# Kernel optimization log

Measured on AMD Instinct MI355X. Metric: run time of the kernel, lower is better.

The kernel has to match this reference:

```python
import jax, jax.numpy as jnp
import numpy as np

VOCAB = 65
N_EMBED = 256
BLOCK = 32
N_HEAD = 4
N_BLOCKS = 8
HEAD_DIM = N_EMBED // N_HEAD          # 64 (actual projection size)
SCALE = 32 ** (-0.5)                   # source bug: scales by GLOBAL head_size=32
LN_EPS = 1e-5


def _layer_norm(x, g, b):
    m = jnp.mean(x, axis=-1, keepdims=True)
    v = jnp.mean((x - m) ** 2, axis=-1, keepdims=True)
    return (x - m) * jax.lax.rsqrt(v + LN_EPS) * g + b


def setup_inputs() -> dict:
    key = jax.random.key(0)
    ks = jax.random.split(key, 24)
    B, T = 4096, 32
    s = 0.02
    inp = {
        "x": jax.random.randint(ks[0], (B, T), 0, VOCAB),
        "y": jax.random.randint(ks[1], (B, T), 0, VOCAB),
        "tok_table": jax.random.normal(ks[2], (VOCAB, N_EMBED)) * s,
        "pos_table": jax.random.normal(ks[3], (VOCAB, N_EMBED)) * s,
        "Wk": jax.random.normal(ks[4], (N_BLOCKS, N_HEAD, N_EMBED, HEAD_DIM)) * s,
        "Wq": jax.random.normal(ks[5], (N_BLOCKS, N_HEAD, N_EMBED, HEAD_DIM)) * s,
        "Wv": jax.random.normal(ks[6], (N_BLOCKS, N_HEAD, N_EMBED, HEAD_DIM)) * s,
        "Wp": jax.random.normal(ks[7], (N_BLOCKS, N_EMBED, N_EMBED)) * s,
        "bp": jnp.zeros((N_BLOCKS, N_EMBED)),
        "ln1g": jnp.ones((N_BLOCKS, N_EMBED)),
        "ln1b": jnp.zeros((N_BLOCKS, N_EMBED)),
        "W1": jax.random.normal(ks[8], (N_BLOCKS, N_EMBED, 4 * N_EMBED)) * s,
        "b1": jnp.zeros((N_BLOCKS, 4 * N_EMBED)),
        "W2": jax.random.normal(ks[9], (N_BLOCKS, 4 * N_EMBED, N_EMBED)) * s,
        "b2": jnp.zeros((N_BLOCKS, N_EMBED)),
        "ln2g": jnp.ones((N_BLOCKS, N_EMBED)),
        "ln2b": jnp.zeros((N_BLOCKS, N_EMBED)),
        "lmW": jax.random.normal(ks[10], (N_EMBED, VOCAB)) * s,
        "lmb": jnp.zeros((VOCAB,)),
    }
    return inp


def reference(x, y, tok_table, pos_table, Wk, Wq, Wv, Wp, bp, ln1g, ln1b,
              W1, b1, W2, b2, ln2g, ln2b, lmW, lmb):
    B, T = x.shape
    # NOTE: the source indexes the position table with TOKEN ids (a bug we preserve)
    h = tok_table[x] + pos_table[x]                       # [B,T,C]
    tril = jnp.tril(jnp.ones((T, T), dtype=bool))         # [T,T]

    for i in range(N_BLOCKS):
        # --- multi-head attention (scores = k @ q^T, per source) ---
        k = jnp.einsum('btc,hcd->bhtd', h, Wk[i])
        q = jnp.einsum('btc,hcd->bhtd', h, Wq[i])
        v = jnp.einsum('btc,hcd->bhtd', h, Wv[i])
        wei = jnp.einsum('bhtd,bhsd->bhts', k, q) * SCALE  # [B,H,T,T]
        wei = jnp.where(tril[None, None], wei, -jnp.inf)
        wei = jax.nn.softmax(wei, axis=-1)
        attn = jnp.einsum('bhts,bhsd->bhtd', wei, v)       # [B,H,T,Dh]
        attn = attn.transpose(0, 2, 1, 3).reshape(B, T, N_EMBED)
        attn = attn @ Wp[i] + bp[i]
        h = _layer_norm(h + attn, ln1g[i], ln1b[i])
        # --- feed-forward ---
        ff = jax.nn.relu(h @ W1[i] + b1[i]) @ W2[i] + b2[i]
        h = _layer_norm(h + ff, ln2g[i], ln2b[i])

    logits = h @ lmW + lmb                                 # [B,T,V]
    logp = jax.nn.log_softmax(logits, axis=-1)
    loss = -jnp.mean(jnp.take_along_axis(logp, y[..., None], axis=-1))
    return logits, loss
```

## Files before the change

kernel.cpp:

```cpp
#include <hip/hip_runtime.h>
#include <hip/hip_bf16.h>

#define M_TOTAL 131072
#define ATT_SCALE 0.17677669529663687f
#define LN_EPS 1e-5f
#define CDIV(a,b) (((a)+(b)-1)/(b))

using bf16x8 = __attribute__((ext_vector_type(8))) short;
using f32x4  = __attribute__((ext_vector_type(4))) float;

__device__ __forceinline__ float wredsum(float v){
#pragma unroll
  for (int m = 32; m; m >>= 1) v += __shfl_xor(v, m, 64);
  return v;
}

__device__ __forceinline__ unsigned short f2b(float x){
  union { float f; unsigned u; } v; v.f = x;
  unsigned r = v.u + 0x7FFFu + ((v.u >> 16) & 1u);
  return (unsigned short)(r >> 16);
}
__device__ __forceinline__ float b2f(unsigned short u){
  union { unsigned u32; float f; } v; v.u32 = (unsigned)u << 16; return v.f;
}

__global__ void zero1(float* p){ if (threadIdx.x == 0) *p = 0.f; }

__global__ void convert_qkv(const float* __restrict__ Wk, const float* __restrict__ Wq,
                            const float* __restrict__ Wv, unsigned short* __restrict__ WrT){
  int idx = blockIdx.x * 256 + threadIdx.x;
  if (idx >= 8 * 768 * 256) return;
  int k = idx & 255;
  int n = (idx >> 8) % 768;
  int i = idx / (768 * 256);
  int sel = n >> 8, nn = n & 255, hh = nn >> 6, d = nn & 63;
  const float* W = sel == 0 ? Wk : sel == 1 ? Wq : Wv;
  WrT[idx] = f2b(W[((size_t)(i * 4 + hh) * 256 + k) * 64 + d]);
}

__global__ void convert_t(const float* __restrict__ in, unsigned short* __restrict__ outp,
                          int N, int K, int total){
  int idx = blockIdx.x * 256 + threadIdx.x;
  if (idx >= total) return;
  int k = idx % K;
  int n = (idx / K) % N;
  int i = idx / (K * N);
  outp[idx] = f2b(in[((size_t)i * K + k) * N + n]);
}

__global__ void convert_lmw(const float* __restrict__ lmW, const float* __restrict__ lmb,
                            unsigned short* __restrict__ lmWT, float* __restrict__ lmbp){
  int idx = blockIdx.x * 256 + threadIdx.x;
  if (idx >= 80 * 256) return;
  int k = idx & 255, c = idx >> 8;
  lmWT[idx] = (c < 65) ? f2b(lmW[k * 65 + c]) : (unsigned short)0;
  if (idx < 80) lmbp[idx] = (idx < 65) ? lmb[idx] : 0.f;
}

template<bool RELU>
__global__ __launch_bounds__(256)
void gemm_bf(const unsigned short* __restrict__ A, const unsigned short* __restrict__ BT,
             const float* __restrict__ bias, unsigned short* __restrict__ Cb,
             int N, int K){
  __shared__ __align__(16) unsigned short LDS[2][128][64];
  unsigned short (*As)[64] = LDS[0];
  unsigned short (*Bs)[64] = LDS[1];
  const int tid = threadIdx.x;
  const int rowBase = blockIdx.y * 128, colBase = blockIdx.x * 128;
  const int w = tid >> 6, lane = tid & 63;
  const int wm = w >> 1, wn = w & 1;
  const int lm = lane & 15, lk = lane >> 4;

  const int sgrow = w * 32 + (lane >> 3);
  const int sgcol = ((((lane & 7) * 16) ^ ((lane >> 3) << 4)) >> 1);
  const unsigned short* gA = A  + (size_t)(rowBase + sgrow) * K + sgcol;
  const unsigned short* gB = BT + (size_t)(colBase + sgrow) * K + sgcol;

  f32x4 acc[4][4];
#pragma unroll
  for (int m = 0; m < 4; ++m)
#pragma unroll
    for (int n = 0; n < 4; ++n) acc[m][n] = (f32x4){0.f, 0.f, 0.f, 0.f};

  for (int kt = 0; kt < K; kt += 64){
#pragma unroll
    for (int q = 0; q < 4; ++q){
      __builtin_amdgcn_global_load_lds(
        (const __attribute__((address_space(1))) void*)(gA + (size_t)(q * 8) * K + kt),
        (__attribute__((address_space(3))) void*)&As[w * 32 + q * 8][0], 16, 0, 0);
      __builtin_amdgcn_global_load_lds(
        (const __attribute__((address_space(1))) void*)(gB + (size_t)(q * 8) * K + kt),
        (__attribute__((address_space(3))) void*)&Bs[w * 32 + q * 8][0], 16, 0, 0);
    }
    __syncthreads();
#pragma unroll
    for (int half = 0; half < 2; ++half){
      const int cb = (half * 64 + lk * 16) ^ ((lm & 7) << 4);
      bf16x8 a[4], b[4];
#pragma unroll
      for (int m = 0; m < 4; ++m)
        a[m] = *(const bf16x8*)((const char*)&As[wm * 64 + m * 16 + lm][0] + cb);
#pragma unroll
      for (int n = 0; n < 4; ++n)
        b[n] = *(const bf16x8*)((const char*)&Bs[wn * 64 + n * 16 + lm][0] + cb);
#pragma unroll
      for (int m = 0; m < 4; ++m)
#pragma unroll
        for (int n = 0; n < 4; ++n)
          acc[m][n] = __builtin_amdgcn_mfma_f32_16x16x32_bf16(a[m], b[n], acc[m][n], 0, 0, 0);
    }
    __syncthreads();
  }

  unsigned short* bounce = &LDS[0][0][0] + w * 1152;
  const int erow = lane >> 2;
  const int ecol = (lane & 3) * 16;
  const int gc = colBase + wn * 64 + ecol;
#pragma unroll
  for (int m = 0; m < 4; ++m){
#pragma unroll
    for (int n = 0; n < 4; ++n){
      int c = colBase + wn * 64 + n * 16 + lm;
      float bv = bias ? bias[c] : 0.f;
#pragma unroll
      for (int i = 0; i < 4; ++i){
        float v = acc[m][n][i] + bv;
        if (RELU) v = fmaxf(v, 0.f);
        bounce[(lk * 4 + i) * 72 + n * 16 + lm] = f2b(v);
      }
    }
    asm volatile("s_waitcnt lgkmcnt(0)" ::: "memory");
    uint4 v0 = *(const uint4*)&bounce[erow * 72 + ecol];
    uint4 v1 = *(const uint4*)&bounce[erow * 72 + ecol + 8];
    size_t go = (size_t)(rowBase + wm * 64 + m * 16 + erow) * N + gc;
    *(uint4*)(Cb + go)     = v0;
    *(uint4*)(Cb + go + 8) = v1;
  }
}

__global__ void embed_kernel(const int* __restrict__ x, const float* __restrict__ tok,
                             const float* __restrict__ pos, unsigned short* __restrict__ h_bf,
                             int row0, int nrows){
  int total = nrows * 64;
  for (int idx = blockIdx.x * blockDim.x + threadIdx.x; idx < total; idx += gridDim.x * blockDim.x){
    int r = idx >> 6, c4 = (idx & 63) * 4;
    int t = x[row0 + r];
    float4 tv = *(const float4*)(tok + t * 256 + c4);
    float4 pv = *(const float4*)(pos + t * 256 + c4);
    ushort4 o;
    o.x = f2b(tv.x + pv.x); o.y = f2b(tv.y + pv.y);
    o.z = f2b(tv.z + pv.z); o.w = f2b(tv.w + pv.w);
    *(ushort4*)(h_bf + (size_t)r * 256 + c4) = o;
  }
}

__global__ __launch_bounds__(256)
void attn_mfma(const unsigned short* __restrict__ kqv, unsigned short* __restrict__ attn){
  __shared__ __align__(16) unsigned short VT[4][64 * 40];
  __shared__ __align__(16) unsigned short PH[4][32 * 40];
  const int ls = blockIdx.x;
  const int tid = threadIdx.x;
  const int hd = tid >> 6, lane = tid & 63;
  const int lm = lane & 15, lk = lane >> 4;

#pragma unroll
  for (int it = 0; it < 4; ++it){
    int idx = it * 256 + tid;
    int row = idx & 31, col = (idx >> 5) * 8;
    int hh = col >> 6, d = col & 63;
    union { uint4 v4; unsigned short s[8]; } u;
    u.v4 = *(const uint4*)(kqv + (size_t)(ls * 32 + row) * 768 + 512 + col);
#pragma unroll
    for (int j = 0; j < 8; ++j)
      VT[hh][(d + j) * 40 + row] = u.s[j];
  }
  __syncthreads();

  const unsigned short* Kg = kqv + (size_t)(ls * 32) * 768 + hd * 64;
  const unsigned short* Qg = Kg + 256;
  f32x4 sacc[2][2];
#pragma unroll
  for (int m = 0; m < 2; ++m)
#pragma unroll
    for (int n = 0; n < 2; ++n) sacc[m][n] = (f32x4){0.f, 0.f, 0.f, 0.f};
#pragma unroll
  for (int kk = 0; kk < 2; ++kk){
    bf16x8 a[2], b[2];
#pragma unroll
    for (int m = 0; m < 2; ++m)
      a[m] = *(const bf16x8*)(Kg + (size_t)(m * 16 + lm) * 768 + kk * 32 + lk * 8);
#pragma unroll
    for (int n = 0; n < 2; ++n)
      b[n] = *(const bf16x8*)(Qg + (size_t)(n * 16 + lm) * 768 + kk * 32 + lk * 8);
#pragma unroll
    for (int m = 0; m < 2; ++m)
#pragma unroll
      for (int n = 0; n < 2; ++n)
        sacc[m][n] = __builtin_amdgcn_mfma_f32_16x16x32_bf16(a[m], b[n], sacc[m][n], 0, 0, 0);
  }

#pragma unroll
  for (int m = 0; m < 2; ++m){
#pragma unroll
    for (int i = 0; i < 4; ++i){
      int t = m * 16 + lk * 4 + i;
      float v0 = sacc[m][0][i] * ATT_SCALE;
      float v1 = sacc[m][1][i] * ATT_SCALE;
      bool m0 = (lm <= t), m1 = (16 + lm <= t);
      float mx = fmaxf(m0 ? v0 : -1e30f, m1 ? v1 : -1e30f);
#pragma unroll
      for (int msk = 1; msk < 16; msk <<= 1) mx = fmaxf(mx, __shfl_xor(mx, msk, 64));
      float e0 = m0 ? expf(v0 - mx) : 0.f;
      float e1 = m1 ? expf(v1 - mx) : 0.f;
      float sm = e0 + e1;
#pragma unroll
      for (int msk = 1; msk < 16; msk <<= 1) sm += __shfl_xor(sm, msk, 64);
      float inv = 1.f / sm;
      PH[hd][t * 40 + lm]      = f2b(e0 * inv);
      PH[hd][t * 40 + 16 + lm] = f2b(e1 * inv);
    }
  }
  __syncthreads();

  f32x4 pacc[2][4];
  {
    bf16x8 a[2], b[4];
#pragma unroll
    for (int m = 0; m < 2; ++m)
      a[m] = *(const bf16x8*)&PH[hd][(m * 16 + lm) * 40 + lk * 8];
#pragma unroll
    for (int n = 0; n < 4; ++n)
      b[n] = *(const bf16x8*)&VT[hd][(n * 16 + lm) * 40 + lk * 8];
#pragma unroll
    for (int m = 0; m < 2; ++m)
#pragma unroll
      for (int n = 0; n < 4; ++n)
        pacc[m][n] = __builtin_amdgcn_mfma_f32_16x16x32_bf16(
            a[m], b[n], (f32x4){0.f, 0.f, 0.f, 0.f}, 0, 0, 0);
  }

  unsigned short* bounce = &VT[hd][0];
#pragma unroll
  for (int m = 0; m < 2; ++m)
#pragma unroll
    for (int n = 0; n < 4; ++n)
#pragma unroll
      for (int i = 0; i < 4; ++i)
        bounce[(m * 16 + lk * 4 + i) * 72 + n * 16 + lm] = f2b(pacc[m][n][i]);
  asm volatile("s_waitcnt lgkmcnt(0)" ::: "memory");
  const int er = lane >> 1, ec = (lane & 1) * 32;
  size_t gbase = (size_t)(ls * 32 + er) * 256 + hd * 64 + ec;
#pragma unroll
  for (int j = 0; j < 4; ++j)
    *(uint4*)(attn + gbase + j * 8) = *(const uint4*)&bounce[er * 72 + ec + j * 8];
}

__global__ __launch_bounds__(256)
void ln_kernel(unsigned short* __restrict__ h_bf, const unsigned short* __restrict__ po,
               const float* __restrict__ g, const float* __restrict__ b){
  const int w = threadIdx.x >> 6, lane = threadIdx.x & 63;
  const size_t r = (size_t)blockIdx.x * 4 + w;
  const int c4 = lane * 4;
  ushort4 hv = *(const ushort4*)(h_bf + r * 256 + c4);
  ushort4 pv = *(const ushort4*)(po   + r * 256 + c4);
  float v[4];
  v[0] = b2f(hv.x) + b2f(pv.x);
  v[1] = b2f(hv.y) + b2f(pv.y);
  v[2] = b2f(hv.z) + b2f(pv.z);
  v[3] = b2f(hv.w) + b2f(pv.w);
  float s = (v[0] + v[1]) + (v[2] + v[3]);
  s = wredsum(s);
  float mean = s * (1.f / 256.f);
  float q = 0.f;
#pragma unroll
  for (int j = 0; j < 4; ++j){ float d = v[j] - mean; q += d * d; }
  q = wredsum(q);
  float rstd = rsqrtf(q * (1.f / 256.f) + LN_EPS);
  float4 g4 = *(const float4*)(g + c4);
  float4 b4 = *(const float4*)(b + c4);
  ushort4 o;
  o.x = f2b((v[0] - mean) * rstd * g4.x + b4.x);
  o.y = f2b((v[1] - mean) * rstd * g4.y + b4.y);
  o.z = f2b((v[2] - mean) * rstd * g4.z + b4.z);
  o.w = f2b((v[3] - mean) * rstd * g4.w + b4.w);
  *(ushort4*)(h_bf + r * 256 + c4) = o;
}

__global__ __launch_bounds__(256)
void logits_loss_mfma(const unsigned short* __restrict__ h_bf,
                      const unsigned short* __restrict__ lmWT,
                      const float* __restrict__ lmbp, const int* __restrict__ y,
                      float* __restrict__ out, float* __restrict__ partial,
                      int row0){
  __shared__ unsigned short As[64][136];
  __shared__ unsigned short Ws[80][136];
  __shared__ float redw[4];
  const int tid = threadIdx.x;
  const int rowBase = blockIdx.x * 64;
  const int w = tid >> 6, lane = tid & 63;
  const int lm = lane & 15, lk = lane >> 4;

  f32x4 acc[5];
#pragma unroll
  for (int n = 0; n < 5; ++n) acc[n] = (f32x4){0.f, 0.f, 0.f, 0.f};

  for (int kt = 0; kt < 256; kt += 128){
#pragma unroll
    for (int q = 0; q < 4; ++q){
      int idx = tid + 256 * q;
      int r = idx >> 4, k8 = (idx & 15) * 8;
      *(uint4*)&As[r][k8] = *(const uint4*)(h_bf + (size_t)(rowBase + r) * 256 + kt + k8);
    }
#pragma unroll
    for (int q = 0; q < 5; ++q){
      int idx = tid + 256 * q;
      int r = idx >> 4, k8 = (idx & 15) * 8;
      *(uint4*)&Ws[r][k8] = *(const uint4*)(lmWT + (size_t)r * 256 + kt + k8);
    }
    __syncthreads();
#pragma unroll
    for (int kc = 0; kc < 4; ++kc){
      bf16x8 a = *(const bf16x8*)&As[w * 16 + lm][kc * 32 + lk * 8];
#pragma unroll
      for (int n = 0; n < 5; ++n){
        bf16x8 bb = *(const bf16x8*)&Ws[n * 16 + lm][kc * 32 + lk * 8];
        acc[n] = __builtin_amdgcn_mfma_f32_16x16x32_bf16(a, bb, acc[n], 0, 0, 0);
      }
    }
    __syncthreads();
  }

#pragma unroll
  for (int n = 0; n < 5; ++n){
    int c = n * 16 + lm;
    float bv = lmbp[c];
#pragma unroll
    for (int i = 0; i < 4; ++i){
      acc[n][i] += bv;
      if (c < 65){
        int r = rowBase + w * 16 + lk * 4 + i;
        out[(size_t)(row0 + r) * 65 + c] = acc[n][i];
      }
    }
  }

  float nll = 0.f;
#pragma unroll
  for (int i = 0; i < 4; ++i){
    float mx = -1e30f;
#pragma unroll
    for (int n = 0; n < 5; ++n)
      if (n * 16 + lm < 65) mx = fmaxf(mx, acc[n][i]);
#pragma unroll
    for (int mask = 1; mask < 16; mask <<= 1) mx = fmaxf(mx, __shfl_xor(mx, mask, 64));
    float se = 0.f;
#pragma unroll
    for (int n = 0; n < 5; ++n)
      if (n * 16 + lm < 65) se += expf(acc[n][i] - mx);
#pragma unroll
    for (int mask = 1; mask < 16; mask <<= 1) se += __shfl_xor(se, mask, 64);
    float lse = mx + logf(se);
    int gr = rowBase + w * 16 + lk * 4 + i;
    int yv = y[row0 + gr];
    float ly = 0.f;
#pragma unroll
    for (int n = 0; n < 5; ++n)
      if (n * 16 + lm == yv) ly = acc[n][i];
#pragma unroll
    for (int mask = 1; mask < 16; mask <<= 1) ly += __shfl_xor(ly, mask, 64);
    nll += lse - ly;
  }
  if (lm != 0) nll = 0.f;
  nll += __shfl_xor(nll, 16, 64);
  nll += __shfl_xor(nll, 32, 64);
  if (lane == 0) redw[w] = nll;
  __syncthreads();
  if (tid == 0) partial[blockIdx.x] = redw[0] + redw[1] + redw[2] + redw[3];
}

__global__ __launch_bounds__(256)
void loss_red(const float* __restrict__ partial, int n, float* __restrict__ loss_sum){
  __shared__ float red[256];
  float s = 0.f;
  for (int i = threadIdx.x; i < n; i += 256) s += partial[i];
  red[threadIdx.x] = s;
  __syncthreads();
  for (int st = 128; st; st >>= 1){
    if (threadIdx.x < st) red[threadIdx.x] += red[threadIdx.x + st];
    __syncthreads();
  }
  if (threadIdx.x == 0) *loss_sum += red[0];
}

__global__ void loss_fin(const float* __restrict__ loss_sum, float* __restrict__ out){
  if (threadIdx.x == 0)
    out[(size_t)M_TOTAL * 65] = *loss_sum * (1.f / (float)M_TOTAL);
}

extern "C" void kernel_launch(void* const* d_in, const int* in_sizes, int n_in,
                              void* d_out, int out_size, void* d_ws, size_t ws_size,
                              hipStream_t stream) {
  const int*   x    = (const int*)  d_in[0];
  const int*   y    = (const int*)  d_in[1];
  const float* tok  = (const float*)d_in[2];
  const float* pos  = (const float*)d_in[3];
  const float* Wk   = (const float*)d_in[4];
  const float* Wq   = (const float*)d_in[5];
  const float* Wv   = (const float*)d_in[6];
  const float* Wp   = (const float*)d_in[7];
  const float* bp   = (const float*)d_in[8];
  const float* ln1g = (const float*)d_in[9];
  const float* ln1b = (const float*)d_in[10];
  const float* W1   = (const float*)d_in[11];
  const float* b1   = (const float*)d_in[12];
  const float* W2   = (const float*)d_in[13];
  const float* b2   = (const float*)d_in[14];
  const float* ln2g = (const float*)d_in[15];
  const float* ln2b = (const float*)d_in[16];
  const float* lmW  = (const float*)d_in[17];
  const float* lmb  = (const float*)d_in[18];
  float* out = (float*)d_out;

  float* loss_sum = (float*)d_ws;
  float* partial  = loss_sum + 64;
  unsigned short* lmWT = (unsigned short*)(partial + 1024);
  float* lmbp = (float*)(lmWT + 80 * 256);
  unsigned short* WrT = (unsigned short*)(lmbp + 80);
  unsigned short* WpT = WrT + (size_t)8 * 768 * 256;
  unsigned short* W1T = WpT + (size_t)8 * 256 * 256;
  unsigned short* W2T = W1T + (size_t)8 * 1024 * 256;
  unsigned short* bufs = W2T + (size_t)8 * 256 * 1024;
  size_t fixed = (size_t)(64 + 1024) * 4 + (size_t)80 * 256 * 2 + 80 * 4 +
                 ((size_t)8 * 768 * 256 + 8 * 256 * 256 + 8 * 1024 * 256 + 8 * 256 * 1024) * 2;
  const size_t per_row = (size_t)(768 + 256 + 256 + 1024) * 2;
  size_t avail = ws_size > fixed ? ws_size - fixed : 0;
  long rmax = (long)(avail / per_row) & ~255L;
  if (rmax < 256) rmax = 256;
  int R = (int)(rmax < (long)M_TOTAL ? rmax : (long)M_TOTAL);

  unsigned short* kqv_b  = bufs;
  unsigned short* h_bf   = kqv_b  + (size_t)R * 768;
  unsigned short* attn_b = h_bf   + (size_t)R * 256;
  unsigned short* ff1_b  = attn_b + (size_t)R * 256;
  unsigned short* po_b = kqv_b;

  zero1<<<1, 64, 0, stream>>>(loss_sum);
  convert_qkv<<<CDIV(8 * 768 * 256, 256), 256, 0, stream>>>(Wk, Wq, Wv, WrT);
  convert_t<<<CDIV(8 * 256 * 256, 256), 256, 0, stream>>>(Wp, WpT, 256, 256, 8 * 256 * 256);
  convert_t<<<CDIV(8 * 1024 * 256, 256), 256, 0, stream>>>(W1, W1T, 1024, 256, 8 * 1024 * 256);
  convert_t<<<CDIV(8 * 256 * 1024, 256), 256, 0, stream>>>(W2, W2T, 256, 1024, 8 * 256 * 1024);
  convert_lmw<<<80, 256, 0, stream>>>(lmW, lmb, lmWT, lmbp);

  for (int row0 = 0; row0 < M_TOTAL; row0 += R){
    int nr = (M_TOTAL - row0) < R ? (M_TOTAL - row0) : R;
    int eg = CDIV(nr * 64, 256); if (eg > 4096) eg = 4096;
    embed_kernel<<<eg, 256, 0, stream>>>(x, tok, pos, h_bf, row0, nr);
    for (int i = 0; i < 8; ++i){
      gemm_bf<false><<<dim3(6, nr / 128), 256, 0, stream>>>(
          h_bf, WrT + (size_t)i * 768 * 256, nullptr, kqv_b, 768, 256);
      attn_mfma<<<nr / 32, 256, 0, stream>>>(kqv_b, attn_b);
      gemm_bf<false><<<dim3(2, nr / 128), 256, 0, stream>>>(
          attn_b, WpT + (size_t)i * 256 * 256, bp + i * 256, po_b, 256, 256);
      ln_kernel<<<nr / 4, 256, 0, stream>>>(h_bf, po_b, ln1g + i * 256, ln1b + i * 256);
      gemm_bf<true><<<dim3(8, nr / 128), 256, 0, stream>>>(
          h_bf, W1T + (size_t)i * 1024 * 256, b1 + i * 1024, ff1_b, 1024, 256);
      gemm_bf<false><<<dim3(2, nr / 128), 256, 0, stream>>>(
          ff1_b, W2T + (size_t)i * 256 * 1024, b2 + i * 256, po_b, 256, 1024);
      ln_kernel<<<nr / 4, 256, 0, stream>>>(h_bf, po_b, ln2g + i * 256, ln2b + i * 256);
    }
    logits_loss_mfma<<<nr / 64, 256, 0, stream>>>(h_bf, lmWT, lmbp, y, out, partial, row0);
    loss_red<<<1, 256, 0, stream>>>(partial, nr / 64, loss_sum);
  }
  loss_fin<<<1, 64, 0, stream>>>(loss_sum, out);
}
```

Measured before the change: 5.607 ms.

## Fuse output projection and FFN down GEMMs with residual add and LayerNorm

Adds a gemm_ln kernel in which one 512-thread block computes full 256-column rows for 128 rows, then adds bias and residual and does the LayerNorm in-block using shuffles plus shared-memory reductions. It replaces the two-launch pattern of gemm_bf followed by ln_kernel for both the attention projection and the FFN down projection. This removes the round-trip of the projected output through global memory and one launch per use, 16 launches per chunk in total. In exchange the grid shrinks to nr/128 blocks with no double buffering, the kernel uses more registers, and the residual read and the output write use scalar 2-byte accesses.

```diff
diff --git a/kernel.cpp b/kernel.cpp
--- a/kernel.cpp
+++ b/kernel.cpp
@@ -138,6 +138,148 @@
   }
 }
 
+__global__ __launch_bounds__(512)
+void gemm_ln(const unsigned short* __restrict__ A, const unsigned short* __restrict__ BT,
+             const float* __restrict__ bias, unsigned short* __restrict__ h_bf,
+             const float* __restrict__ g, const float* __restrict__ b, int K){
+  __shared__ unsigned short As[128][72];
+  __shared__ unsigned short Bs[256][72];
+  __shared__ float redA[4][128];
+  __shared__ float redB[4][128];
+  const int tid = threadIdx.x;
+  const int rowBase = blockIdx.x * 128;
+  const int w = tid >> 6, lane = tid & 63;
+  const int wm = w >> 2, wn = w & 3;
+  const int lm = lane & 15, lk = lane >> 4;
+  const int srow = tid >> 3, scol = (tid & 7) * 8;
+
+  f32x4 acc[4][4];
+#pragma unroll
+  for (int m = 0; m < 4; ++m)
+#pragma unroll
+    for (int n = 0; n < 4; ++n) acc[m][n] = (f32x4){0.f, 0.f, 0.f, 0.f};
+
+  for (int kt = 0; kt < K; kt += 64){
+#pragma unroll
+    for (int q = 0; q < 2; ++q){
+      int r = srow + 64 * q;
+      *(uint4*)&As[r][scol] = *(const uint4*)(A + (size_t)(rowBase + r) * K + kt + scol);
+    }
+#pragma unroll
+    for (int q = 0; q < 4; ++q){
+      int r = srow + 64 * q;
+      *(uint4*)&Bs[r][scol] = *(const uint4*)(BT + (size_t)r * K + kt + scol);
+    }
+    __syncthreads();
+#pragma unroll
+    for (int half = 0; half < 2; ++half){
+      bf16x8 a[4], b8[4];
+#pragma unroll
+      for (int m = 0; m < 4; ++m)
+        a[m] = *(const bf16x8*)&As[wm * 64 + m * 16 + lm][half * 32 + lk * 8];
+#pragma unroll
+      for (int n = 0; n < 4; ++n)
+        b8[n] = *(const bf16x8*)&Bs[wn * 64 + n * 16 + lm][half * 32 + lk * 8];
+#pragma unroll
+      for (int m = 0; m < 4; ++m)
+#pragma unroll
+        for (int n = 0; n < 4; ++n)
+          acc[m][n] = __builtin_amdgcn_mfma_f32_16x16x32_bf16(a[m], b8[n], acc[m][n], 0, 0, 0);
+    }
+    __syncthreads();
+  }
+
+  float gg[4], bb[4], bv[4];
+#pragma unroll
+  for (int n = 0; n < 4; ++n){
+    int c = wn * 64 + n * 16 + lm;
+    bv[n] = bias[c]; gg[n] = g[c]; bb[n] = b[c];
+  }
+#pragma unroll
+  for (int m = 0; m < 4; ++m)
+#pragma unroll
+    for (int i = 0; i < 4; ++i){
+      size_t rr = (size_t)(rowBase + wm * 64 + m * 16 + lk * 4 + i) * 256;
+#pragma unroll
+      for (int n = 0; n < 4; ++n)
+        acc[m][n][i] += bv[n] + b2f(h_bf[rr + wn * 64 + n * 16 + lm]);
+    }
+
+  float pr[4][4];
+#pragma unroll
+  for (int m = 0; m < 4; ++m)
+#pragma unroll
+    for (int i = 0; i < 4; ++i)
+      pr[m][i] = acc[m][0][i] + acc[m][1][i] + acc[m][2][i] + acc[m][3][i];
+#pragma unroll
+  for (int mask = 1; mask < 16; mask <<= 1)
+#pragma unroll
+    for (int m = 0; m < 4; ++m)
+#pragma unroll
+      for (int i = 0; i < 4; ++i)
+        pr[m][i] += __shfl_xor(pr[m][i], mask, 64);
+  if (lm == 0){
+#pragma unroll
+    for (int m = 0; m < 4; ++m)
+#pragma unroll
+      for (int i = 0; i < 4; ++i)
+        redA[wn][wm * 64 + m * 16 + lk * 4 + i] = pr[m][i];
+  }
+  __syncthreads();
+  float mean[4][4];
+#pragma unroll
+  for (int m = 0; m < 4; ++m)
+#pragma unroll
+    for (int i = 0; i < 4; ++i){
+      int lr = wm * 64 + m * 16 + lk * 4 + i;
+      mean[m][i] = (redA[0][lr] + redA[1][lr] + redA[2][lr] + redA[3][lr]) * (1.f / 256.f);
+    }
+
+#pragma unroll
+  for (int m = 0; m < 4; ++m)
+#pragma unroll
+    for (int i = 0; i < 4; ++i){
+      float q = 0.f;
+#pragma unroll
+      for (int n = 0; n < 4; ++n){
+        float d = acc[m][n][i] - mean[m][i];
+        q += d * d;
+      }
+      pr[m][i] = q;
+    }
+#pragma unroll
+  for (int mask = 1; mask < 16; mask <<= 1)
+#pragma unroll
+    for (int m = 0; m < 4; ++m)
+#pragma unroll
+      for (int i = 0; i < 4; ++i)
+        pr[m][i] += __shfl_xor(pr[m][i], mask, 64);
+  if (lm == 0){
+#pragma unroll
+    for (int m = 0; m < 4; ++m)
+#pragma unroll
+      for (int i = 0; i < 4; ++i)
+        redB[wn][wm * 64 + m * 16 + lk * 4 + i] = pr[m][i];
+  }
+  __syncthreads();
+
+#pragma unroll
+  for (int m = 0; m < 4; ++m)
+#pragma unroll
+    for (int i = 0; i < 4; ++i){
+      int lr = wm * 64 + m * 16 + lk * 4 + i;
+      float var = (redB[0][lr] + redB[1][lr] + redB[2][lr] + redB[3][lr]) * (1.f / 256.f);
+      float rstd = rsqrtf(var + LN_EPS);
+      size_t rr = (size_t)(rowBase + lr) * 256;
+#pragma unroll
+      for (int n = 0; n < 4; ++n){
+        int c = wn * 64 + n * 16 + lm;
+        float nv = (acc[m][n][i] - mean[m][i]) * rstd * gg[n] + bb[n];
+        h_bf[rr + c] = f2b(nv);
+      }
+    }
+}
+
 __global__ void embed_kernel(const int* __restrict__ x, const float* __restrict__ tok,
                              const float* __restrict__ pos, unsigned short* __restrict__ h_bf,
                              int row0, int nrows){
@@ -253,37 +395,6 @@
 #pragma unroll
   for (int j = 0; j < 4; ++j)
     *(uint4*)(attn + gbase + j * 8) = *(const uint4*)&bounce[er * 72 + ec + j * 8];
-}
-
-__global__ __launch_bounds__(256)
-void ln_kernel(unsigned short* __restrict__ h_bf, const unsigned short* __restrict__ po,
-               const float* __restrict__ g, const float* __restrict__ b){
-  const int w = threadIdx.x >> 6, lane = threadIdx.x & 63;
-  const size_t r = (size_t)blockIdx.x * 4 + w;
-  const int c4 = lane * 4;
-  ushort4 hv = *(const ushort4*)(h_bf + r * 256 + c4);
-  ushort4 pv = *(const ushort4*)(po   + r * 256 + c4);
-  float v[4];
-  v[0] = b2f(hv.x) + b2f(pv.x);
-  v[1] = b2f(hv.y) + b2f(pv.y);
-  v[2] = b2f(hv.z) + b2f(pv.z);
-  v[3] = b2f(hv.w) + b2f(pv.w);
-  float s = (v[0] + v[1]) + (v[2] + v[3]);
-  s = wredsum(s);
-  float mean = s * (1.f / 256.f);
-  float q = 0.f;
-#pragma unroll
-  for (int j = 0; j < 4; ++j){ float d = v[j] - mean; q += d * d; }
-  q = wredsum(q);
-  float rstd = rsqrtf(q * (1.f / 256.f) + LN_EPS);
-  float4 g4 = *(const float4*)(g + c4);
-  float4 b4 = *(const float4*)(b + c4);
-  ushort4 o;
-  o.x = f2b((v[0] - mean) * rstd * g4.x + b4.x);
-  o.y = f2b((v[1] - mean) * rstd * g4.y + b4.y);
-  o.z = f2b((v[2] - mean) * rstd * g4.z + b4.z);
-  o.w = f2b((v[3] - mean) * rstd * g4.w + b4.w);
-  *(ushort4*)(h_bf + r * 256 + c4) = o;
 }
 
 __global__ __launch_bounds__(256)
@@ -442,7 +553,6 @@
   unsigned short* h_bf   = kqv_b  + (size_t)R * 768;
   unsigned short* attn_b = h_bf   + (size_t)R * 256;
   unsigned short* ff1_b  = attn_b + (size_t)R * 256;
-  unsigned short* po_b = kqv_b;
 
   zero1<<<1, 64, 0, stream>>>(loss_sum);
   convert_qkv<<<CDIV(8 * 768 * 256, 256), 256, 0, stream>>>(Wk, Wq, Wv, WrT);
@@ -459,14 +569,14 @@
       gemm_bf<false><<<dim3(6, nr / 128), 256, 0, stream>>>(
           h_bf, WrT + (size_t)i * 768 * 256, nullptr, kqv_b, 768, 256);
       attn_mfma<<<nr / 32, 256, 0, stream>>>(kqv_b, attn_b);
-      gemm_bf<false><<<dim3(2, nr / 128), 256, 0, stream>>>(
-          attn_b, WpT + (size_t)i * 256 * 256, bp + i * 256, po_b, 256, 256);
-      ln_kernel<<<nr / 4, 256, 0, stream>>>(h_bf, po_b, ln1g + i * 256, ln1b + i * 256);
+      gemm_ln<<<nr / 128, 512, 0, stream>>>(
+          attn_b, WpT + (size_t)i * 256 * 256, bp + i * 256, h_bf,
+          ln1g + i * 256, ln1b + i * 256, 256);
       gemm_bf<true><<<dim3(8, nr / 128), 256, 0, stream>>>(
           h_bf, W1T + (size_t)i * 1024 * 256, b1 + i * 1024, ff1_b, 1024, 256);
-      gemm_bf<false><<<dim3(2, nr / 128), 256, 0, stream>>>(
-          ff1_b, W2T + (size_t)i * 256 * 1024, b2 + i * 256, po_b, 256, 1024);
-      ln_kernel<<<nr / 4, 256, 0, stream>>>(h_bf, po_b, ln2g + i * 256, ln2b + i * 256);
+      gemm_ln<<<nr / 128, 512, 0, stream>>>(
+          ff1_b, W2T + (size_t)i * 256 * 1024, b2 + i * 256, h_bf,
+          ln2g + i * 256, ln2b + i * 256, 1024);
     }
     logits_loss_mfma<<<nr / 64, 256, 0, stream>>>(h_bf, lmWT, lmbp, y, out, partial, row0);
     loss_red<<<1, 256, 0, stream>>>(partial, nr / 64, loss_sum);
```

Result: slower. 6.107 ms (median of 4 runs) (+8.9%).
